# Kernel optimization log

Hardware: AMD Instinct MI355X
Metric: run time of the kernel (lower is better)

The kernel has to match this reference:

```python
import jax, jax.numpy as jnp
import numpy as np

STRIDE = 4
EPS = 1e-12  # guards sqrt grad at exactly-zero distance (weight[0] is all zeros)


def rbf_conv(x, w, stride=STRIDE):
    # x: (N, 1, H, W); w: (O, kh, kw). Computes per-window cdist to all O
    # prototype filters, then gauss RBF with std = unbiased std of the (N, O)
    # distance matrix at each window position (matches torch.std(dist)).
    O, kh, kw = w.shape
    patches = jax.lax.conv_general_dilated_patches(
        x, (kh, kw), (stride, stride), 'VALID')      # (N, kh*kw, oh, ow)
    p = jnp.transpose(patches, (0, 2, 3, 1))          # (N, oh, ow, P)
    wf = w.reshape(O, -1)                              # (O, P)
    d2 = (jnp.sum(p * p, -1)[..., None] + jnp.sum(wf * wf, -1)
          - 2.0 * jnp.einsum('nhwp,op->nhwo', p, wf))
    dist = jnp.sqrt(jnp.maximum(d2, 0.0) + EPS)       # (N, oh, ow, O)
    std = jnp.std(dist, axis=(0, 3), ddof=1, keepdims=True)  # per window pos
    out = jnp.exp(-0.5 * (dist / std) ** 2)           # gauss RBF
    return jnp.transpose(out, (0, 3, 1, 2))           # (N, O, oh, ow)


def crelu(x, b):
    return x * (x >= b).astype(x.dtype)


def sfm(x, shape, next_kernel, filt, alpha0=0.9):
    # get_RM: (N, C, h_in, w_in) -> (B, h, w, C) regrouping, then alpha-weighted
    # patch pooling over `filt`, emitting (B*h'*w', 1, kh_next, kw_next).
    h, w = shape
    f0, f1 = filt
    C = x.shape[1]
    rm = jnp.transpose(x, (0, 2, 3, 1)).reshape(-1, h, w, C)
    seq = jnp.arange(f0 * f1, dtype=x.dtype)[::-1]       # flipped sequence
    alpha = jnp.tile((alpha0 ** seq).reshape(f0, f1), (h // f0, w // f1))
    out = rm * alpha[None, :, :, None]
    out = out.reshape(-1, h // f0, f0, w // f1, f1, C).mean(axis=(2, 4))
    return out.reshape(-1, 1, *next_kernel)


def channel_forward(xc, w1, w2, w3, w4, cb):
    y = rbf_conv(xc, w1)                       # (B, 100, 6, 6)
    y = crelu(y, cb[0])
    y = sfm(y, (6, 6), (10, 10), (2, 2))       # (B*9, 1, 10, 10)
    y = rbf_conv(y, w2)                        # (B*9, 225, 1, 1)
    y = crelu(y, cb[1])
    y = sfm(y, (3, 3), (15, 15), (1, 3))       # (B*3, 1, 15, 15)
    y = rbf_conv(y, w3)                        # (B*3, 625, 1, 1)
    y = crelu(y, cb[2])
    y = sfm(y, (3, 1), (25, 25), (3, 1))       # (B, 1, 25, 25)
    y = rbf_conv(y, w4)                        # (B, 1225, 1, 1)
    y = crelu(y, cb[3])
    return y


def forward(x, w1, w2, w3, w4, fc_w, fc_b, crelu_bias):
    B = x.shape[0]
    feats = [channel_forward(x[:, c:c + 1], w1[c], w2[c], w3[c], w4[c], crelu_bias)
             for c in range(x.shape[1])]        # fixed loop over 3 color channels
    out = jnp.concatenate(feats, axis=1).reshape(B, -1)  # (B, 3*1225)
    return out @ fc_w.T + fc_b


def setup_inputs() -> dict:
    key = jax.random.key(0)
    ks = jax.random.split(key, 8)

    def kaiming_u(k, shape):
        fan_in = int(np.prod(shape[2:]))        # 1*kh*kw, matches torch
        bound = float(np.sqrt(1.0 / fan_in))    # kaiming_uniform(a=sqrt(5))
        w = jax.random.uniform(k, shape, jnp.float32, -bound, bound)
        return w.at[:, 0].set(0.0)              # torch init zeros filter 0

    B = 4096
    return {
        'x': jax.random.uniform(ks[0], (B, 3, 28, 28), jnp.float32),
        'w1': kaiming_u(ks[1], (3, 100, 5, 5)),
        'w2': kaiming_u(ks[2], (3, 225, 10, 10)),
        'w3': kaiming_u(ks[3], (3, 625, 15, 15)),
        'w4': kaiming_u(ks[4], (3, 1225, 25, 25)),
        'fc_w': jax.random.normal(ks[5], (10, 3 * 1225), jnp.float32) * 0.016,
        'fc_b': jnp.zeros((10,), jnp.float32),
        'crelu_bias': jnp.array([0.4, 0.1, 0.01, 0.01], jnp.float32),
    }


def reference(x, w1, w2, w3, w4, fc_w, fc_b, crelu_bias):
    return forward(x, w1, w2, w3, w4, fc_w, fc_b, crelu_bias)
```

## Files before the change

### kernel.cpp

```cpp
#include <hip/hip_runtime.h>


typedef unsigned short u16;
typedef short bf16x8 __attribute__((ext_vector_type(8)));
typedef float f32x4 __attribute__((ext_vector_type(4)));
typedef unsigned int u32;
typedef u32 u32x4 __attribute__((ext_vector_type(4)));

#define STRIPES 64
#define ACC_L2 0
#define ACC_L3 128
#define ACC_L4 256
#define ACC_TOTAL 384

__device__ __forceinline__ u16 f2bf(float f) {
  unsigned int u = __float_as_uint(f);
  unsigned int r = (u + 0x7fffu + ((u >> 16) & 1u)) >> 16;
  return (u16)r;
}
__device__ __forceinline__ float bf2f(u16 h) {
  return __uint_as_float(((unsigned int)h) << 16);
}
__device__ __forceinline__ u32 cvtpk_bf16(float a, float b) {
  u32 r;
  asm("v_cvt_pk_bf16_f32 %0, %1, %2" : "=v"(r) : "v"(a), "v"(b));
  return r;
}
__device__ __forceinline__ float fexp(float x) { return __expf(x); }
__device__ __forceinline__ float fsqrt(float x) { return __builtin_amdgcn_sqrtf(x); }
__device__ __forceinline__ void gload16(const void* g, const void* l) {
  __builtin_amdgcn_global_load_lds(
      (const __attribute__((address_space(1))) unsigned int*)g,
      (__attribute__((address_space(3))) unsigned int*)l, 16, 0, 0);
}

__global__ void zero_acc_kernel(double* __restrict__ acc, int n) {
  int i = blockIdx.x * blockDim.x + threadIdx.x;
  if (i < n) acc[i] = 0.0;
}

__global__ __launch_bounds__(128) void w_prep(
    const float* __restrict__ W, int O, int K, int Opad, int Kp,
    u16* __restrict__ hi, u16* __restrict__ lo, float* __restrict__ wn)
{
  __shared__ float red[2];
  int o = blockIdx.x, cc = blockIdx.y, t = threadIdx.x;
  const float* src = W + ((size_t)cc * O + o) * K;
  u16* dh = hi + ((size_t)cc * Opad + o) * Kp;
  u16* dl = lo + ((size_t)cc * Opad + o) * Kp;
  float p = 0.f;
  for (int k = t; k < Kp; k += 128) {
    float v = (o < O && k < K) ? src[k] : 0.f;
    u16 h = f2bf(v);
    u16 l = f2bf(v - bf2f(h));
    dh[k] = h; dl[k] = l;
    p = fmaf(v, v, p);
  }
  for (int off = 32; off; off >>= 1) p += __shfl_down(p, off, 64);
  if ((t & 63) == 0) red[t >> 6] = p;
  __syncthreads();
  if (t == 0) wn[(size_t)cc * Opad + o] = red[0] + red[1];
}

__global__ __launch_bounds__(256) void l1_gemm_d2(
    const float* __restrict__ x, int c0,
    const u16* __restrict__ W1h, const u16* __restrict__ W1l,
    const float* __restrict__ w1n, float* __restrict__ dist1, int sD1c,
    float* __restrict__ part, int sPartc, int NBLK)
{
  __shared__ __align__(16) u16 sm[16384];
  __shared__ float img[1568];
  __shared__ float pnsm[512];
  __shared__ float pnloc[128];
  const int t = threadIdx.x;
  const int w = t >> 6, lane = t & 63;
  const int b0 = blockIdx.x * 2;
  const int zi = blockIdx.y, c = c0 + zi;
  const u16* Wh = W1h + (size_t)c * 4096;
  const u16* Wl = W1l + (size_t)c * 4096;
  const float* wn = w1n + (size_t)c * 128;
  dist1 += (size_t)zi * sD1c;
  part  += (size_t)zi * sPartc;

  {
    const int kk = (w & 3) * 8;
#pragma unroll
    for (int u = 0; u < 2; ++u) {
      const size_t gb = (size_t)(u * 64 + lane) * 32 + kk;
      const int ls = ((w & 3) * 128 + u * 64) * 8;
      gload16(Wh + gb, sm + 8192 + ls);
      gload16(Wl + gb, sm + 12288 + ls);
    }
  }
#pragma unroll
  for (int im = 0; im < 2; ++im) {
    if (t < 196)
      ((float4*)(img + im * 784))[t] =
          ((const float4*)(x + ((size_t)(b0 + im) * 3 + c) * 784))[t];
  }
// ... 125 lines not shown
    inv36[pos] = var > 0.0 ? (float)(0.5 / var) : __builtin_inff();
  }
}

__global__ __launch_bounds__(128) void l1_sfm_lite(
    const float* __restrict__ d1, int sD1c,
    const float* __restrict__ inv36, int sInvc, const float* __restrict__ cb,
    u16* __restrict__ Xhi, u16* __restrict__ Xlo, float* __restrict__ xn,
    int sXc, int sxnc)
{
  __shared__ float inv_s[36];
  __shared__ float xnsm[9][2];
  int b = blockIdx.x, zi = blockIdx.y, t = threadIdx.x;
  d1 += (size_t)zi * sD1c; inv36 += (size_t)zi * sInvc;
  Xhi += (size_t)zi * sXc; Xlo += (size_t)zi * sXc; xn += (size_t)zi * sxnc;
  if (t < 36) inv_s[t] = inv36[t];
  __syncthreads();
  const float* db = d1 + (size_t)b * 3600;
  float bias = cb[0];
  int wv = t >> 6;
#pragma unroll
  for (int IJ = 0; IJ < 9; ++IJ) {
    const int I = IJ / 3, J = IJ - I * 3;
    const int p00 = 12 * I + 2 * J;
    float v = 0.f;
    if (t < 100) {
      float e00 = fexp(-db[p00 * 100 + t] * inv_s[p00]);
      float e01 = fexp(-db[(p00 + 1) * 100 + t] * inv_s[p00 + 1]);
      float e10 = fexp(-db[(p00 + 6) * 100 + t] * inv_s[p00 + 6]);
      float e11 = fexp(-db[(p00 + 7) * 100 + t] * inv_s[p00 + 7]);
      e00 = (e00 >= bias) ? e00 : 0.f;
      e01 = (e01 >= bias) ? e01 : 0.f;
      e10 = (e10 >= bias) ? e10 : 0.f;
      e11 = (e11 >= bias) ? e11 : 0.f;
      v = 0.25f * (fmaf(0.729f, e00, 0.81f * e01) + fmaf(0.9f, e10, e11));
    }
    size_t xrow = (size_t)b * 9 + IJ;
    u16 h = f2bf(v);
    u16 l = f2bf(v - bf2f(h));
    Xhi[xrow * 128 + t] = h;
    Xlo[xrow * 128 + t] = l;
    float p = v * v;
    for (int off = 32; off; off >>= 1) p += __shfl_down(p, off, 64);
    if ((t & 63) == 0) xnsm[IJ][wv] = p;
  }
  __syncthreads();
  if (t < 9) xn[(size_t)b * 9 + t] = xnsm[t][0] + xnsm[t][1];
}

__global__ __launch_bounds__(512, 2) void gemm_dist_pipe(
    const u16* __restrict__ Xhi, const u16* __restrict__ Xlo,
    const u16* __restrict__ Whi, const u16* __restrict__ Wlo,
    const float* __restrict__ xn, const float* __restrict__ wn,
    float* __restrict__ dist, int O, int Kp,
    double* __restrict__ acc, int accbase, int c0,
    int sXc, int sWc, int sxnc, int swnc, int sdistc)
{
  __shared__ __align__(16) u16 sm[65536];
  int zi = blockIdx.z, c = c0 + zi;
  Xhi += (size_t)zi * sXc; Xlo += (size_t)zi * sXc;
  Whi += (size_t)c * sWc;  Wlo += (size_t)c * sWc;
  xn += (size_t)zi * sxnc; wn += (size_t)c * swnc;
  dist += (size_t)zi * sdistc;
  acc += (size_t)c * ACC_TOTAL;

  const int t = threadIdx.x;
  const int w = t >> 6, lane = t & 63;
  const int wr = w >> 1, wc = w & 1;
  const int sq = w & 3, half = w >> 2;
  const int m0 = blockIdx.x * 256, o0 = blockIdx.y * 256;
  const int q4 = lane >> 4, r16 = lane & 15;
  const int nsteps = Kp / 32;

  f32x4 accv[4][8];
#pragma unroll
  for (int i = 0; i < 4; ++i)
#pragma unroll
    for (int j = 0; j < 8; ++j) accv[i][j] = (f32x4){0.f, 0.f, 0.f, 0.f};

  auto stageA_u = [&](int buf, int ks, int u) {
    const int kk = ks * 32 + sq * 8;
    u16* base = sm + buf * 32768;
    const int row = half * 128 + u * 64 + lane;
    const size_t ga = (size_t)(m0 + row) * Kp + kk;
    const int ls = (sq * 256 + half * 128 + u * 64) * 8;
    gload16(Xhi + ga, base + ls);
    gload16(Xlo + ga, base + 8192 + ls);
  };
  auto stageB_u = [&](int buf, int ks, int u) {
    const int kk = ks * 32 + sq * 8;
    u16* base = sm + buf * 32768;
    const int row = half * 128 + u * 64 + lane;
    const size_t gb = (size_t)(o0 + row) * Kp + kk;
    const int ls = (sq * 256 + half * 128 + u * 64) * 8;
    gload16(Whi + gb, base + 16384 + ls);
    gload16(Wlo + gb, base + 24576 + ls);
  };

  stageA_u(0, 0, 0); stageA_u(0, 0, 1);
  stageB_u(0, 0, 0); stageB_u(0, 0, 1);

  for (int ks = 0; ks < nsteps; ++ks) {
    const u16* base = sm + (ks & 1) * 32768;
    const int nb = (ks + 1) & 1;
    const bool more = (ks + 1 < nsteps);
    bf16x8 Ah[4], Al[4];

#pragma unroll
    for (int ph = 0; ph < 4; ++ph) {
      if (ph == 0) {
        asm volatile("s_waitcnt vmcnt(2)\n\ts_barrier" ::: "memory");
      } else if (ph == 2) {
        if (more) asm volatile("s_waitcnt vmcnt(4)\n\ts_barrier" ::: "memory");
        else      asm volatile("s_waitcnt vmcnt(0)\n\ts_barrier" ::: "memory");
      } else {
        __builtin_amdgcn_s_barrier();
      }
      if (ph == 0) {
#pragma unroll
        for (int i = 0; i < 4; ++i) {
          int ao = (q4 * 256 + wr * 64 + i * 16 + r16) * 8;
          Ah[i] = *(const bf16x8*)(base + ao);
          Al[i] = *(const bf16x8*)(base + 8192 + ao);
        }
      }
      const int j0 = ph * 2;
      int bo0 = (q4 * 256 + wc * 128 + j0 * 16 + r16) * 8;
      int bo1 = (q4 * 256 + wc * 128 + (j0 + 1) * 16 + r16) * 8;
      bf16x8 Bh0 = *(const bf16x8*)(base + 16384 + bo0);
      bf16x8 Bl0 = *(const bf16x8*)(base + 24576 + bo0);
      bf16x8 Bh1 = *(const bf16x8*)(base + 16384 + bo1);
      bf16x8 Bl1 = *(const bf16x8*)(base + 24576 + bo1);
      if (more) {
        if (ph == 0)      stageA_u(nb, ks + 1, 0);
        else if (ph == 1) stageA_u(nb, ks + 1, 1);
        else if (ph == 2) stageB_u(nb, ks + 1, 0);
        else              stageB_u(nb, ks + 1, 1);
      }
      asm volatile("s_waitcnt lgkmcnt(0)" ::: "memory");
      __builtin_amdgcn_sched_barrier(0);
      __builtin_amdgcn_s_setprio(1);
#pragma unroll
      for (int i = 0; i < 4; ++i)
        accv[i][j0] = __builtin_amdgcn_mfma_f32_16x16x32_bf16(Ah[i], Bh0, accv[i][j0], 0, 0, 0);
#pragma unroll
      for (int i = 0; i < 4; ++i)
        accv[i][j0] = __builtin_amdgcn_mfma_f32_16x16x32_bf16(Al[i], Bh0, accv[i][j0], 0, 0, 0);
#pragma unroll
      for (int i = 0; i < 4; ++i)
        accv[i][j0] = __builtin_amdgcn_mfma_f32_16x16x32_bf16(Ah[i], Bl0, accv[i][j0], 0, 0, 0);
#pragma unroll
      for (int i = 0; i < 4; ++i)
        accv[i][j0 + 1] = __builtin_amdgcn_mfma_f32_16x16x32_bf16(Ah[i], Bh1, accv[i][j0 + 1], 0, 0, 0);
#pragma unroll
      for (int i = 0; i < 4; ++i)
        accv[i][j0 + 1] = __builtin_amdgcn_mfma_f32_16x16x32_bf16(Al[i], Bh1, accv[i][j0 + 1], 0, 0, 0);
#pragma unroll
      for (int i = 0; i < 4; ++i)
        accv[i][j0 + 1] = __builtin_amdgcn_mfma_f32_16x16x32_bf16(Ah[i], Bl1, accv[i][j0 + 1], 0, 0, 0);
      __builtin_amdgcn_s_setprio(0);
    }
  }

  double s = 0.0, qd = 0.0;
#pragma unroll
  for (int i = 0; i < 4; ++i) {
    const int mb = m0 + wr * 64 + i * 16 + q4 * 4;
    float xnv[4];
#pragma unroll
    for (int r = 0; r < 4; ++r) xnv[r] = xn[mb + r];
    float sf = 0.f, qf = 0.f;
#pragma unroll
    for (int j = 0; j < 8; ++j) {
      const int o = o0 + wc * 128 + j * 16 + r16;
      if (o < O) {
        const float wnv = wn[o];
#pragma unroll
        for (int r = 0; r < 4; ++r) {
          float d2 = xnv[r] + wnv - 2.f * accv[i][j][r];
          float d2c = fmaxf(d2, 0.f) + 1e-12f;
          dist[(size_t)(mb + r) * O + o] = d2c;
          sf += fsqrt(d2c); qf += d2c;
        }
      }
    }
    s += sf; qd += qf;
  }
  for (int off = 32; off; off >>= 1) {
    s += __shfl_down(s, off, 64);
    qd += __shfl_down(qd, off, 64);
  }
  double* redsm = (double*)(sm + (nsteps & 1) * 32768);
  if (lane == 0) { redsm[w * 2] = s; redsm[w * 2 + 1] = qd; }
  __syncthreads();
  if (t == 0) {
    s = 0.0; qd = 0.0;
#pragma unroll
    for (int ww = 0; ww < 8; ++ww) { s += redsm[ww * 2]; qd += redsm[ww * 2 + 1]; }
    int stripe = (blockIdx.x + blockIdx.y * gridDim.x) & (STRIPES - 1);
    atomicAdd(&acc[accbase + stripe * 2], s);
    atomicAdd(&acc[accbase + stripe * 2 + 1], qd);
  }
}

__device__ __forceinline__ float block_inv_from_acc(
    const double* __restrict__ acc, int base, double n, float* sh)
{
  __syncthreads();
  int t = threadIdx.x;
  if (t < 64) {
    double s = acc[base + 2 * t], q = acc[base + 2 * t + 1];
    for (int off = 32; off; off >>= 1) {
      s += __shfl_down(s, off, 64);
      q += __shfl_down(q, off, 64);
    }
    if (t == 0) {
      double var = (q - s * s / n) / (n - 1.0);
      *sh = var > 0.0 ? (float)(0.5 / var) : __builtin_inff();
    }
  }
  __syncthreads();
  return *sh;
}

__global__ __launch_bounds__(256) void l2_sfm(
    const float* __restrict__ dist2, const double* __restrict__ acc, double n,
    const float* __restrict__ cb, u16* __restrict__ Xhi, u16* __restrict__ Xlo,
    float* __restrict__ xn, int c0, int sdistc, int sXc, int sxnc)
{
  __shared__ float shinv;
  __shared__ float red[4];
  int zi = blockIdx.z, c = c0 + zi;
  dist2 += (size_t)zi * sdistc;
  Xhi += (size_t)zi * sXc; Xlo += (size_t)zi * sXc; xn += (size_t)zi * sxnc;
  float inv = block_inv_from_acc(acc + (size_t)c * ACC_TOTAL, ACC_L2, n, &shinv);
  int b = blockIdx.x, u = blockIdx.y, ch = threadIdx.x;
  float bias = cb[1];
  float v = 0.f;
  if (ch < 225) {
    const float av[3] = {0.81f, 0.9f, 1.0f};
    float a = 0.f;
#pragma unroll
    for (int vv = 0; vv < 3; ++vv) {
      float d2 = dist2[((size_t)b * 9 + u * 3 + vv) * 225 + ch];
      float e = fexp(-d2 * inv);
      e = (e >= bias) ? e : 0.f;
      a = fmaf(e, av[vv], a);
    }
    v = a * (1.f / 3.f);
  }
  size_t row = (size_t)b * 3 + u;
  u16 h = f2bf(v);
  u16 l = f2bf(v - bf2f(h));
  Xhi[row * 256 + ch] = h;
  Xlo[row * 256 + ch] = l;
  float p = v * v;
  for (int off = 32; off; off >>= 1) p += __shfl_down(p, off, 64);
  if ((ch & 63) == 0) red[ch >> 6] = p;
  __syncthreads();
  if (ch == 0) xn[row] = red[0] + red[1] + red[2] + red[3];
}

__global__ __launch_bounds__(256) void l3_sfm(
    const float* __restrict__ dist3, const double* __restrict__ acc, double n,
    const float* __restrict__ cb, u16* __restrict__ Xhi, u16* __restrict__ Xlo,
    float* __restrict__ xn, int c0, int sdistc, int sXc, int sxnc)
{
  __shared__ float shinv;
  __shared__ float red[4];
  int zi = blockIdx.y, c = c0 + zi;
  dist3 += (size_t)zi * sdistc;
  Xhi += (size_t)zi * sXc; Xlo += (size_t)zi * sXc; xn += (size_t)zi * sxnc;
  float inv = block_inv_from_acc(acc + (size_t)c * ACC_TOTAL, ACC_L3, n, &shinv);
  int b = blockIdx.x, t = threadIdx.x;
  float bias = cb[2];
  const float au[3] = {0.81f, 0.9f, 1.0f};
  float p = 0.f;
  for (int ch = t; ch < 640; ch += 256) {
    float v = 0.f;
    if (ch < 625) {
      float a = 0.f;
#pragma unroll
      for (int u = 0; u < 3; ++u) {
        float d2 = dist3[((size_t)b * 3 + u) * 625 + ch];
        float e = fexp(-d2 * inv);
        e = (e >= bias) ? e : 0.f;
        a = fmaf(e, au[u], a);
      }
      v = a * (1.f / 3.f);
    }
    u16 h = f2bf(v);
    u16 l = f2bf(v - bf2f(h));
    Xhi[(size_t)b * 640 + ch] = h;
    Xlo[(size_t)b * 640 + ch] = l;
    p = fmaf(v, v, p);
  }
  for (int off = 32; off; off >>= 1) p += __shfl_down(p, off, 64);
  if ((t & 63) == 0) red[t >> 6] = p;
  __syncthreads();
  if (t == 0) xn[b] = red[0] + red[1] + red[2] + red[3];
}

__global__ __launch_bounds__(128) void fc_acc(
    const float* __restrict__ dist4, const double* __restrict__ acc, double n,
    const float* __restrict__ cb, const float* __restrict__ fcw,
    const float* __restrict__ fcb, float* __restrict__ out,
    int c0, int nc, int sdistc)
{
  __shared__ float shinv;
  int b = blockIdx.x, t = threadIdx.x;
  float bias = cb[3];
  float p[10];
#pragma unroll
  for (int k = 0; k < 10; ++k) p[k] = 0.f;
  for (int zi = 0; zi < nc; ++zi) {
    int c = c0 + zi;
    float inv = block_inv_from_acc(acc + (size_t)c * ACC_TOTAL, ACC_L4, n, &shinv);
    const float* d4 = dist4 + (size_t)zi * sdistc;
    for (int j = t; j < 1225; j += 128) {
      float d2 = d4[(size_t)b * 1225 + j];
      float v = fexp(-d2 * inv);
      v = (v >= bias) ? v : 0.f;
#pragma unroll
      for (int k = 0; k < 10; ++k) p[k] = fmaf(v, fcw[k * 3675 + c * 1225 + j], p[k]);
    }
  }
#pragma unroll
  for (int k = 0; k < 10; ++k)
    for (int off = 32; off; off >>= 1) p[k] += __shfl_down(p[k], off, 64);
  __shared__ float red[2][10];
  int wave = t >> 6;
  if ((t & 63) == 0) {
#pragma unroll
    for (int k = 0; k < 10; ++k) red[wave][k] = p[k];
  }
  __syncthreads();
  if (t < 10) {
    float v = red[0][t] + red[1][t];
    if (c0 == 0) out[(size_t)b * 10 + t] = fcb[t] + v;
    else         out[(size_t)b * 10 + t] += v;
  }
}

extern "C" void kernel_launch(void* const* d_in, const int* in_sizes, int n_in,
                              void* d_out, int out_size, void* d_ws, size_t ws_size,
                              hipStream_t stream) {
  const float* x   = (const float*)d_in[0];
  const float* w1  = (const float*)d_in[1];
  const float* w2  = (const float*)d_in[2];
  const float* w3  = (const float*)d_in[3];
  const float* w4  = (const float*)d_in[4];
  const float* fcw = (const float*)d_in[5];
  const float* fcb = (const float*)d_in[6];
  const float* cb  = (const float*)d_in[7];
  float* out = (float*)d_out;
  const int B = in_sizes[0] / (3 * 28 * 28);
  const int M2 = B * 9, M3 = B * 3;
  const int NB = B / 2;

  const size_t W2SZ = 256 * 128, W3SZ = 768 * 256, W4SZ = (size_t)1280 * 640;
  const size_t WTOT = 3 * (W2SZ + W3SZ + W4SZ);

  int tier;
  u16 *Xbase, *Whi, *Wlo, *W1h, *W1l;
  float *wn, *w1n, *xn, *inv36, *part;
  double* accd;
  float* Sf;
  for (tier = 0; tier < 3; ++tier) {
    size_t cur = 0;
    char* basep = (char*)d_ws;
    auto take = [&](size_t bytes) {
      void* r = basep + cur;
      cur = (cur + bytes + 255) & ~(size_t)255;
      return r;
    };
    int nc = (tier <= 1) ? 3 : 1;
    int ncL1 = (tier == 0) ? 3 : 1;
    size_t Ssz = (size_t)M2 * 225 * 4 * nc;
    size_t d1sz = (size_t)B * 3600 * 4 * ncL1;
    if (d1sz > Ssz) Ssz = d1sz;
    Sf = (float*)take(Ssz);
    Xbase = (u16*)take((size_t)M2 * 128 * 2 * 2 * nc);
    Whi = (u16*)take(WTOT * 2); Wlo = (u16*)take(WTOT * 2);
    W1h = (u16*)take(12288 * 2); W1l = (u16*)take(12288 * 2);
    wn  = (float*)take(3 * (256 + 768 + 1280) * 4);
    w1n = (float*)take(384 * 4);
    xn    = (float*)take((size_t)M2 * 4 * nc);
    inv36 = (float*)take(40 * 4 * ncL1);
    part  = (float*)take((size_t)72 * NB * 4 * ncL1);
    accd  = (double*)take(3 * ACC_TOTAL * 8);
    if (cur <= ws_size || tier == 2) break;
  }
  const int nc = (tier <= 1) ? 3 : 1;
  const bool batL1 = (tier == 0);

  const int sX2c   = (nc == 3) ? M2 * 128 * 2 : 0;
  const int sX3c   = (nc == 3) ? M3 * 256 * 2 : 0;
  const int sX4c   = (nc == 3) ? B * 640 * 2 : 0;
  const int sD2c   = (nc == 3) ? M2 * 225 : 0;
  const int sD3c   = (nc == 3) ? M3 * 625 : 0;
  const int sD4c   = (nc == 3) ? B * 1225 : 0;
  const int sXn2c  = (nc == 3) ? M2 : 0;
  const int sXn3c  = (nc == 3) ? M3 : 0;
  const int sXn4c  = (nc == 3) ? B : 0;
  const int sD1c   = batL1 ? B * 3600 : 0;
  const int sPartc = batL1 ? 72 * NB : 0;
  const int sInvL1 = batL1 ? 40 : 0;

  u16* x2hi = Xbase;   u16* x2lo = Xbase + (size_t)M2 * 128;
  u16* x3hi = Xbase;   u16* x3lo = Xbase + (size_t)M3 * 256;
  u16* x4hi = Xbase;   u16* x4lo = Xbase + (size_t)B * 640;
  u16* Whi2 = Whi;                 u16* Wlo2 = Wlo;                 float* wn2 = wn;
  u16* Whi3 = Whi + 3 * W2SZ;      u16* Wlo3 = Wlo + 3 * W2SZ;      float* wn3 = wn + 3 * 256;
  u16* Whi4 = Whi + 3 * (W2SZ + W3SZ); u16* Wlo4 = Wlo + 3 * (W2SZ + W3SZ);
  float* wn4 = wn + 3 * (256 + 768);

  zero_acc_kernel<<<(3 * ACC_TOTAL + 255) / 256, 256, 0, stream>>>(accd, 3 * ACC_TOTAL);
  w_prep<<<dim3(128, 3),  128, 0, stream>>>(w1, 100, 25,  128, 32,  W1h,  W1l,  w1n);
  w_prep<<<dim3(256, 3),  128, 0, stream>>>(w2, 225, 100, 256, 128, Whi2, Wlo2, wn2);
  w_prep<<<dim3(768, 3),  128, 0, stream>>>(w3, 625, 225, 768, 256, Whi3, Wlo3, wn3);
  w_prep<<<dim3(1280, 3), 128, 0, stream>>>(w4, 1225, 625, 1280, 640, Whi4, Wlo4, wn4);

  for (int c0 = 0; c0 < 3; c0 += nc) {
    if (batL1) {
      l1_gemm_d2<<<dim3(NB, 3), 256, 0, stream>>>(x, 0, W1h, W1l, w1n, Sf, sD1c,
                                                  part, sPartc, NB);
      l1_part_fin<<<dim3(36, 3), 256, 0, stream>>>(part, sPartc, inv36, sInvL1,
                                                   (double)B * 100.0, NB);
      l1_sfm_lite<<<dim3(B, 3), 128, 0, stream>>>(
          Sf, sD1c, inv36, sInvL1, cb, x2hi, x2lo, xn, sX2c, sXn2c);
    } else {
      for (int ci = 0; ci < nc; ++ci) {
        int c = c0 + ci;
        l1_gemm_d2<<<dim3(NB, 1), 256, 0, stream>>>(x, c, W1h, W1l, w1n, Sf, 0,
                                                    part, 0, NB);
        l1_part_fin<<<dim3(36, 1), 256, 0, stream>>>(part, 0, inv36, 0,
                                                     (double)B * 100.0, NB);
        l1_sfm_lite<<<dim3(B, 1), 128, 0, stream>>>(
            Sf, 0, inv36, 0, cb, x2hi + (size_t)ci * sX2c, x2lo + (size_t)ci * sX2c,
            xn + (size_t)ci * sXn2c, 0, 0);
      }
    }

    gemm_dist_pipe<<<dim3(M2 / 256, 1, nc), 512, 0, stream>>>(
        x2hi, x2lo, Whi2, Wlo2, xn, wn2, Sf, 225, 128, accd, ACC_L2, c0,
        sX2c, (int)W2SZ, sXn2c, 256, sD2c);
    l2_sfm<<<dim3(B, 3, nc), 256, 0, stream>>>(
        Sf, accd, (double)M2 * 225.0, cb, x3hi, x3lo, xn, c0, sD2c, sX3c, sXn3c);

    gemm_dist_pipe<<<dim3(M3 / 256, 3, nc), 512, 0, stream>>>(
        x3hi, x3lo, Whi3, Wlo3, xn, wn3, Sf, 625, 256, accd, ACC_L3, c0,
        sX3c, (int)W3SZ, sXn3c, 768, sD3c);
    l3_sfm<<<dim3(B, nc), 256, 0, stream>>>(
        Sf, accd, (double)M3 * 625.0, cb, x4hi, x4lo, xn, c0, sD3c, sX4c, sXn4c);

    gemm_dist_pipe<<<dim3(B / 256, 5, nc), 512, 0, stream>>>(
        x4hi, x4lo, Whi4, Wlo4, xn, wn4, Sf, 1225, 640, accd, ACC_L4, c0,
        sX4c, (int)W4SZ, sXn4c, 1280, sD4c);
    fc_acc<<<B, 128, 0, stream>>>(
        Sf, accd, (double)B * 1225.0, cb, fcw, fcb, out, c0, nc, sD4c);
  }
}
```

Before: 479.7 us.

## Fuse layer-4 distance GEMM with FC via cooperative grid sync; merge prep kernels

```diff
diff --git a/kernel.cpp b/kernel.cpp
--- a/kernel.cpp
+++ b/kernel.cpp
@@ -1,5 +1,8 @@
 #include <hip/hip_runtime.h>
-
+#include <hip/hip_cooperative_groups.h>
+
+
+namespace cg = cooperative_groups;
 
 typedef unsigned short u16;
 typedef short bf16x8 __attribute__((ext_vector_type(8)));
@@ -34,17 +37,31 @@
       (__attribute__((address_space(3))) unsigned int*)l, 16, 0, 0);
 }
 
-__global__ void zero_acc_kernel(double* __restrict__ acc, int n) {
-  int i = blockIdx.x * blockDim.x + threadIdx.x;
-  if (i < n) acc[i] = 0.0;
-}
-
-__global__ __launch_bounds__(128) void w_prep(
-    const float* __restrict__ W, int O, int K, int Opad, int Kp,
-    u16* __restrict__ hi, u16* __restrict__ lo, float* __restrict__ wn)
+__global__ __launch_bounds__(128) void prep_all(
+    const float* __restrict__ w1, const float* __restrict__ w2,
+    const float* __restrict__ w3, const float* __restrict__ w4,
+    u16* __restrict__ W1h, u16* __restrict__ W1l,
+    u16* __restrict__ Whi2, u16* __restrict__ Wlo2,
+    u16* __restrict__ Whi3, u16* __restrict__ Wlo3,
+    u16* __restrict__ Whi4, u16* __restrict__ Wlo4,
+    float* __restrict__ w1n, float* __restrict__ wn2,
+    float* __restrict__ wn3, float* __restrict__ wn4,
+    double* __restrict__ accd, int naccd)
 {
   __shared__ float red[2];
-  int o = blockIdx.x, cc = blockIdx.y, t = threadIdx.x;
+  int bid = blockIdx.x, t = threadIdx.x;
+  if (bid < 9) {
+    int i = bid * 128 + t;
+    if (i < naccd) accd[i] = 0.0;
+    return;
+  }
+  bid -= 9;
+  const float* W; u16 *hi, *lo; float* wn; int O, K, Opad, Kp;
+  if (bid < 384)        { W = w1; hi = W1h;  lo = W1l;  wn = w1n; O = 100;  K = 25;  Opad = 128;  Kp = 32;  }
+  else if (bid < 1152)  { bid -= 384;  W = w2; hi = Whi2; lo = Wlo2; wn = wn2; O = 225;  K = 100; Opad = 256;  Kp = 128; }
+  else if (bid < 3456)  { bid -= 1152; W = w3; hi = Whi3; lo = Wlo3; wn = wn3; O = 625;  K = 225; Opad = 768;  Kp = 256; }
+  else                  { bid -= 3456; W = w4; hi = Whi4; lo = Wlo4; wn = wn4; O = 1225; K = 625; Opad = 1280; Kp = 640; }
+  int o = bid % Opad, cc = bid / Opad;
   const float* src = W + ((size_t)cc * O + o) * K;
   u16* dh = hi + ((size_t)cc * Opad + o) * Kp;
   u16* dl = lo + ((size_t)cc * Opad + o) * Kp;
@@ -447,6 +464,213 @@
   return *sh;
 }
 
+__global__ __launch_bounds__(512, 2) void gemm4_fc_coop(
+    const u16* __restrict__ Xhi, const u16* __restrict__ Xlo,
+    const u16* __restrict__ Whi, const u16* __restrict__ Wlo,
+    const float* __restrict__ xn, const float* __restrict__ wn,
+    const float* __restrict__ fcw, const float* __restrict__ cb,
+    float* __restrict__ part4, int O, int Kp,
+    double* __restrict__ acc, int accbase, int c0,
+    int sXc, int sWc, int sxnc, int swnc, double nsum)
+{
+  __shared__ __align__(16) u16 sm[65536];
+  __shared__ float shinv;
+  int zi = blockIdx.z, c = c0 + zi;
+  Xhi += (size_t)zi * sXc; Xlo += (size_t)zi * sXc;
+  Whi += (size_t)c * sWc;  Wlo += (size_t)c * sWc;
+  xn += (size_t)zi * sxnc; wn += (size_t)c * swnc;
+  double* accl = acc + (size_t)c * ACC_TOTAL;
+
+  const int t = threadIdx.x;
+  const int w = t >> 6, lane = t & 63;
+  const int wr = w >> 1, wc = w & 1;
+  const int sq = w & 3, half = w >> 2;
+  const int m0 = blockIdx.x * 256, o0 = blockIdx.y * 256;
+  const int q4 = lane >> 4, r16 = lane & 15;
+  const int nsteps = Kp / 32;
+  const int B = gridDim.x * 256;
+
+  f32x4 accv[4][8];
+#pragma unroll
+  for (int i = 0; i < 4; ++i)
+#pragma unroll
+    for (int j = 0; j < 8; ++j) accv[i][j] = (f32x4){0.f, 0.f, 0.f, 0.f};
+
+  auto stageA_u = [&](int buf, int ks, int u) {
+    const int kk = ks * 32 + sq * 8;
+    u16* base = sm + buf * 32768;
+    const int row = half * 128 + u * 64 + lane;
+    const size_t ga = (size_t)(m0 + row) * Kp + kk;
+    const int ls = (sq * 256 + half * 128 + u * 64) * 8;
+    gload16(Xhi + ga, base + ls);
+    gload16(Xlo + ga, base + 8192 + ls);
+  };
+  auto stageB_u = [&](int buf, int ks, int u) {
+    const int kk = ks * 32 + sq * 8;
+    u16* base = sm + buf * 32768;
+    const int row = half * 128 + u * 64 + lane;
+    const size_t gb = (size_t)(o0 + row) * Kp + kk;
+    const int ls = (sq * 256 + half * 128 + u * 64) * 8;
+    gload16(Whi + gb, base + 16384 + ls);
+    gload16(Wlo + gb, base + 24576 + ls);
+  };
+
+  stageA_u(0, 0, 0); stageA_u(0, 0, 1);
+  stageB_u(0, 0, 0); stageB_u(0, 0, 1);
+
+  for (int ks = 0; ks < nsteps; ++ks) {
+    const u16* base = sm + (ks & 1) * 32768;
+    const int nb = (ks + 1) & 1;
+    const bool more = (ks + 1 < nsteps);
+    bf16x8 Ah[4], Al[4];
+
+#pragma unroll
+    for (int ph = 0; ph < 4; ++ph) {
+      if (ph == 0) {
+        asm volatile("s_waitcnt vmcnt(2)\n\ts_barrier" ::: "memory");
+      } else if (ph == 2) {
+        if (more) asm volatile("s_waitcnt vmcnt(4)\n\ts_barrier" ::: "memory");
+        else      asm volatile("s_waitcnt vmcnt(0)\n\ts_barrier" ::: "memory");
+      } else {
+        __builtin_amdgcn_s_barrier();
+      }
+      if (ph == 0) {
+#pragma unroll
+        for (int i = 0; i < 4; ++i) {
+          int ao = (q4 * 256 + wr * 64 + i * 16 + r16) * 8;
+          Ah[i] = *(const bf16x8*)(base + ao);
+          Al[i] = *(const bf16x8*)(base + 8192 + ao);
+        }
+      }
+      const int j0 = ph * 2;
+      int bo0 = (q4 * 256 + wc * 128 + j0 * 16 + r16) * 8;
+      int bo1 = (q4 * 256 + wc * 128 + (j0 + 1) * 16 + r16) * 8;
+      bf16x8 Bh0 = *(const bf16x8*)(base + 16384 + bo0);
+      bf16x8 Bl0 = *(const bf16x8*)(base + 24576 + bo0);
+      bf16x8 Bh1 = *(const bf16x8*)(base + 16384 + bo1);
+      bf16x8 Bl1 = *(const bf16x8*)(base + 24576 + bo1);
+      if (more) {
+        if (ph == 0)      stageA_u(nb, ks + 1, 0);
+        else if (ph == 1) stageA_u(nb, ks + 1, 1);
+        else if (ph == 2) stageB_u(nb, ks + 1, 0);
+        else              stageB_u(nb, ks + 1, 1);
+      }
+      asm volatile("s_waitcnt lgkmcnt(0)" ::: "memory");
+      __builtin_amdgcn_sched_barrier(0);
+      __builtin_amdgcn_s_setprio(1);
+#pragma unroll
+      for (int i = 0; i < 4; ++i)
+        accv[i][j0] = __builtin_amdgcn_mfma_f32_16x16x32_bf16(Ah[i], Bh0, accv[i][j0], 0, 0, 0);
+#pragma unroll
+      for (int i = 0; i < 4; ++i)
+        accv[i][j0] = __builtin_amdgcn_mfma_f32_16x16x32_bf16(Al[i], Bh0, accv[i][j0], 0, 0, 0);
+#pragma unroll
+      for (int i = 0; i < 4; ++i)
+        accv[i][j0] = __builtin_amdgcn_mfma_f32_16x16x32_bf16(Ah[i], Bl0, accv[i][j0], 0, 0, 0);
+#pragma unroll
+      for (int i = 0; i < 4; ++i)
+        accv[i][j0 + 1] = __builtin_amdgcn_mfma_f32_16x16x32_bf16(Ah[i], Bh1, accv[i][j0 + 1], 0, 0, 0);
+#pragma unroll
+      for (int i = 0; i < 4; ++i)
+        accv[i][j0 + 1] = __builtin_amdgcn_mfma_f32_16x16x32_bf16(Al[i], Bh1, accv[i][j0 + 1], 0, 0, 0);
+#pragma unroll
+      for (int i = 0; i < 4; ++i)
+        accv[i][j0 + 1] = __builtin_amdgcn_mfma_f32_16x16x32_bf16(Ah[i], Bl1, accv[i][j0 + 1], 0, 0, 0);
+      __builtin_amdgcn_s_setprio(0);
+    }
+  }
+
+  double s = 0.0, qd = 0.0;
+#pragma unroll
+  for (int i = 0; i < 4; ++i) {
+    const int mb = m0 + wr * 64 + i * 16 + q4 * 4;
+    float xnv[4];
+#pragma unroll
+    for (int r = 0; r < 4; ++r) xnv[r] = xn[mb + r];
+    float sf = 0.f, qf = 0.f;
+#pragma unroll
+    for (int j = 0; j < 8; ++j) {
+      const int o = o0 + wc * 128 + j * 16 + r16;
+      const float wnv = (o < 1280) ? wn[o] : 0.f;
+#pragma unroll
+      for (int r = 0; r < 4; ++r) {
+        float d2 = xnv[r] + wnv - 2.f * accv[i][j][r];
+        float d2c = fmaxf(d2, 0.f) + 1e-12f;
+        accv[i][j][r] = d2c;
+        if (o < O) { sf += fsqrt(d2c); qf += d2c; }
+      }
+    }
+    s += sf; qd += qf;
+  }
+  for (int off = 32; off; off >>= 1) {
+    s += __shfl_down(s, off, 64);
+    qd += __shfl_down(qd, off, 64);
+  }
+  double* redsm = (double*)(sm + (nsteps & 1) * 32768);
+  if (lane == 0) { redsm[w * 2] = s; redsm[w * 2 + 1] = qd; }
+  __syncthreads();
+  if (t == 0) {
+    s = 0.0; qd = 0.0;
+#pragma unroll
+    for (int ww = 0; ww < 8; ++ww) { s += redsm[ww * 2]; qd += redsm[ww * 2 + 1]; }
+    int stripe = (blockIdx.x + blockIdx.y * gridDim.x) & (STRIPES - 1);
+    atomicAdd(&accl[accbase + stripe * 2], s);
+    atomicAdd(&accl[accbase + stripe * 2 + 1], qd);
+  }
+
+  cg::this_grid().sync();
+
+  float inv = block_inv_from_acc(accl, accbase, nsum, &shinv);
+  float bias = cb[3];
+#pragma unroll
+  for (int i = 0; i < 4; ++i)
+#pragma unroll
+    for (int j = 0; j < 8; ++j)
+#pragma unroll
+      for (int r = 0; r < 4; ++r) {
+        float v = fexp(-accv[i][j][r] * inv);
+        accv[i][j][r] = (v >= bias) ? v : 0.f;
+      }
+
+  for (int k = 0; k < 10; ++k) {
+    float w8[8];
+#pragma unroll
+    for (int j = 0; j < 8; ++j) {
+      int o = o0 + wc * 128 + j * 16 + r16;
+      w8[j] = (o < O) ? fcw[(size_t)k * 3675 + c * 1225 + o] : 0.f;
+    }
+#pragma unroll
+    for (int i = 0; i < 4; ++i) {
+#pragma unroll
+      for (int r = 0; r < 4; ++r) {
+        float ps = 0.f;
+#pragma unroll
+        for (int j = 0; j < 8; ++j) ps = fmaf(accv[i][j][r], w8[j], ps);
+#pragma unroll
+        for (int off = 8; off; off >>= 1) ps += __shfl_xor(ps, off, 64);
+        if (r16 == 0) {
+          int b = m0 + wr * 64 + i * 16 + q4 * 4 + r;
+          part4[((((size_t)zi * 5 + blockIdx.y) * 2 + wc) * B + b) * 10 + k] = ps;
+        }
+      }
+    }
+  }
+}
+
+__global__ __launch_bounds__(640) void fc_fin(
+    const float* __restrict__ part4, const float* __restrict__ fcb,
+    float* __restrict__ out, int c0, int nc, int B)
+{
+  int b = blockIdx.x * 64 + threadIdx.x / 10;
+  int k = threadIdx.x % 10;
+  float s = (c0 == 0) ? fcb[k] : out[(size_t)b * 10 + k];
+  for (int zi = 0; zi < nc; ++zi)
+#pragma unroll
+    for (int ob = 0; ob < 10; ++ob)
+      s += part4[((((size_t)zi * 5) + (ob >> 1)) * 2 + (ob & 1)) * (size_t)B * 10 + (size_t)b * 10 + k];
+  out[(size_t)b * 10 + k] = s;
+}
+
 __global__ __launch_bounds__(256) void l2_sfm(
     const float* __restrict__ dist2, const double* __restrict__ acc, double n,
     const float* __restrict__ cb, u16* __restrict__ Xhi, u16* __restrict__ Xlo,
@@ -523,47 +747,6 @@
   if ((t & 63) == 0) red[t >> 6] = p;
   __syncthreads();
   if (t == 0) xn[b] = red[0] + red[1] + red[2] + red[3];
-}
-
-__global__ __launch_bounds__(128) void fc_acc(
-    const float* __restrict__ dist4, const double* __restrict__ acc, double n,
-    const float* __restrict__ cb, const float* __restrict__ fcw,
-    const float* __restrict__ fcb, float* __restrict__ out,
-    int c0, int nc, int sdistc)
-{
-  __shared__ float shinv;
-  int b = blockIdx.x, t = threadIdx.x;
-  float bias = cb[3];
-  float p[10];
-#pragma unroll
-  for (int k = 0; k < 10; ++k) p[k] = 0.f;
-  for (int zi = 0; zi < nc; ++zi) {
-    int c = c0 + zi;
-    float inv = block_inv_from_acc(acc + (size_t)c * ACC_TOTAL, ACC_L4, n, &shinv);
-    const float* d4 = dist4 + (size_t)zi * sdistc;
-    for (int j = t; j < 1225; j += 128) {
-      float d2 = d4[(size_t)b * 1225 + j];
-      float v = fexp(-d2 * inv);
-      v = (v >= bias) ? v : 0.f;
-#pragma unroll
-      for (int k = 0; k < 10; ++k) p[k] = fmaf(v, fcw[k * 3675 + c * 1225 + j], p[k]);
-    }
-  }
-#pragma unroll
-  for (int k = 0; k < 10; ++k)
-    for (int off = 32; off; off >>= 1) p[k] += __shfl_down(p[k], off, 64);
-  __shared__ float red[2][10];
-  int wave = t >> 6;
-  if ((t & 63) == 0) {
-#pragma unroll
-    for (int k = 0; k < 10; ++k) red[wave][k] = p[k];
-  }
-  __syncthreads();
-  if (t < 10) {
-    float v = red[0][t] + red[1][t];
-    if (c0 == 0) out[(size_t)b * 10 + t] = fcb[t] + v;
-    else         out[(size_t)b * 10 + t] += v;
-  }
 }
 
 extern "C" void kernel_launch(void* const* d_in, const int* in_sizes, int n_in,
@@ -603,6 +786,8 @@
     size_t Ssz = (size_t)M2 * 225 * 4 * nc;
     size_t d1sz = (size_t)B * 3600 * 4 * ncL1;
     if (d1sz > Ssz) Ssz = d1sz;
+    size_t p4sz = (size_t)nc * 10 * B * 10 * 4;
+    if (p4sz > Ssz) Ssz = p4sz;
     Sf = (float*)take(Ssz);
     Xbase = (u16*)take((size_t)M2 * 128 * 2 * 2 * nc);
     Whi = (u16*)take(WTOT * 2); Wlo = (u16*)take(WTOT * 2);
@@ -623,7 +808,6 @@
   const int sX4c   = (nc == 3) ? B * 640 * 2 : 0;
   const int sD2c   = (nc == 3) ? M2 * 225 : 0;
   const int sD3c   = (nc == 3) ? M3 * 625 : 0;
-  const int sD4c   = (nc == 3) ? B * 1225 : 0;
   const int sXn2c  = (nc == 3) ? M2 : 0;
   const int sXn3c  = (nc == 3) ? M3 : 0;
   const int sXn4c  = (nc == 3) ? B : 0;
@@ -639,11 +823,9 @@
   u16* Whi4 = Whi + 3 * (W2SZ + W3SZ); u16* Wlo4 = Wlo + 3 * (W2SZ + W3SZ);
   float* wn4 = wn + 3 * (256 + 768);
 
-  zero_acc_kernel<<<(3 * ACC_TOTAL + 255) / 256, 256, 0, stream>>>(accd, 3 * ACC_TOTAL);
-  w_prep<<<dim3(128, 3),  128, 0, stream>>>(w1, 100, 25,  128, 32,  W1h,  W1l,  w1n);
-  w_prep<<<dim3(256, 3),  128, 0, stream>>>(w2, 225, 100, 256, 128, Whi2, Wlo2, wn2);
-  w_prep<<<dim3(768, 3),  128, 0, stream>>>(w3, 625, 225, 768, 256, Whi3, Wlo3, wn3);
-  w_prep<<<dim3(1280, 3), 128, 0, stream>>>(w4, 1225, 625, 1280, 640, Whi4, Wlo4, wn4);
+  prep_all<<<9 + 384 + 768 + 2304 + 3840, 128, 0, stream>>>(
+      w1, w2, w3, w4, W1h, W1l, Whi2, Wlo2, Whi3, Wlo3, Whi4, Wlo4,
+      w1n, wn2, wn3, wn4, accd, 3 * ACC_TOTAL);
 
   for (int c0 = 0; c0 < 3; c0 += nc) {
     if (batL1) {
@@ -678,10 +860,23 @@
     l3_sfm<<<dim3(B, nc), 256, 0, stream>>>(
         Sf, accd, (double)M3 * 625.0, cb, x4hi, x4lo, xn, c0, sD3c, sX4c, sXn4c);
 
-    gemm_dist_pipe<<<dim3(B / 256, 5, nc), 512, 0, stream>>>(
-        x4hi, x4lo, Whi4, Wlo4, xn, wn4, Sf, 1225, 640, accd, ACC_L4, c0,
-        sX4c, (int)W4SZ, sXn4c, 1280, sD4c);
-    fc_acc<<<B, 128, 0, stream>>>(
-        Sf, accd, (double)B * 1225.0, cb, fcw, fcb, out, c0, nc, sD4c);
-  }
-}
+    {
+      const u16 *a_xhi = x4hi, *a_xlo = x4lo, *a_whi = Whi4, *a_wlo = Wlo4;
+      const float *a_xn = xn, *a_wn = wn4, *a_fcw = fcw, *a_cb = cb;
+      float* a_part = Sf;
+      int a_O = 1225, a_Kp = 640, a_accbase = ACC_L4, a_c0 = c0;
+      int a_sXc = sX4c, a_sWc = (int)W4SZ, a_sxnc = sXn4c, a_swnc = 1280;
+      double* a_acc = accd;
+      double a_n = (double)B * 1225.0;
+      void* cargs[] = {
+          (void*)&a_xhi, (void*)&a_xlo, (void*)&a_whi, (void*)&a_wlo,
+          (void*)&a_xn, (void*)&a_wn, (void*)&a_fcw, (void*)&a_cb,
+          (void*)&a_part, (void*)&a_O, (void*)&a_Kp, (void*)&a_acc,
+          (void*)&a_accbase, (void*)&a_c0, (void*)&a_sXc, (void*)&a_sWc,
+          (void*)&a_sxnc, (void*)&a_swnc, (void*)&a_n};
+      hipLaunchCooperativeKernel((void*)gemm4_fc_coop, dim3(B / 256, 5, nc),
+                                 dim3(512, 1, 1), cargs, 0, stream);
+    }
+    fc_fin<<<B / 64, 640, 0, stream>>>(Sf, fcb, out, c0, nc, B);
+  }
+}
```

Result: slower. 517.0 us (+7.8%).

## Stage distance tiles through LDS for coalesced padded-row stores; fuse prep kernels

Applied to the files above, without the earlier changes.

```diff
diff --git a/kernel.cpp b/kernel.cpp
--- a/kernel.cpp
+++ b/kernel.cpp
@@ -34,17 +34,31 @@
       (__attribute__((address_space(3))) unsigned int*)l, 16, 0, 0);
 }
 
-__global__ void zero_acc_kernel(double* __restrict__ acc, int n) {
-  int i = blockIdx.x * blockDim.x + threadIdx.x;
-  if (i < n) acc[i] = 0.0;
-}
-
-__global__ __launch_bounds__(128) void w_prep(
-    const float* __restrict__ W, int O, int K, int Opad, int Kp,
-    u16* __restrict__ hi, u16* __restrict__ lo, float* __restrict__ wn)
+__global__ __launch_bounds__(128) void prep_all(
+    const float* __restrict__ w1, const float* __restrict__ w2,
+    const float* __restrict__ w3, const float* __restrict__ w4,
+    u16* __restrict__ W1h, u16* __restrict__ W1l,
+    u16* __restrict__ Whi2, u16* __restrict__ Wlo2,
+    u16* __restrict__ Whi3, u16* __restrict__ Wlo3,
+    u16* __restrict__ Whi4, u16* __restrict__ Wlo4,
+    float* __restrict__ w1n, float* __restrict__ wn2,
+    float* __restrict__ wn3, float* __restrict__ wn4,
+    double* __restrict__ accd, int naccd)
 {
   __shared__ float red[2];
-  int o = blockIdx.x, cc = blockIdx.y, t = threadIdx.x;
+  int bid = blockIdx.x, t = threadIdx.x;
+  if (bid < 9) {
+    int i = bid * 128 + t;
+    if (i < naccd) accd[i] = 0.0;
+    return;
+  }
+  bid -= 9;
+  const float* W; u16 *hi, *lo; float* wn; int O, K, Opad, Kp;
+  if (bid < 384)        { W = w1; hi = W1h;  lo = W1l;  wn = w1n; O = 100;  K = 25;  Opad = 128;  Kp = 32;  }
+  else if (bid < 1152)  { bid -= 384;  W = w2; hi = Whi2; lo = Wlo2; wn = wn2; O = 225;  K = 100; Opad = 256;  Kp = 128; }
+  else if (bid < 3456)  { bid -= 1152; W = w3; hi = Whi3; lo = Wlo3; wn = wn3; O = 625;  K = 225; Opad = 768;  Kp = 256; }
+  else                  { bid -= 3456; W = w4; hi = Whi4; lo = Wlo4; wn = wn4; O = 1225; K = 625; Opad = 1280; Kp = 640; }
+  int o = bid % Opad, cc = bid / Opad;
   const float* src = W + ((size_t)cc * O + o) * K;
   u16* dh = hi + ((size_t)cc * Opad + o) * Kp;
   u16* dl = lo + ((size_t)cc * Opad + o) * Kp;
@@ -276,7 +290,7 @@
     const u16* __restrict__ Xhi, const u16* __restrict__ Xlo,
     const u16* __restrict__ Whi, const u16* __restrict__ Wlo,
     const float* __restrict__ xn, const float* __restrict__ wn,
-    float* __restrict__ dist, int O, int Kp,
+    float* __restrict__ dist, int O, int Od, int Kp,
     double* __restrict__ acc, int accbase, int c0,
     int sXc, int sWc, int sxnc, int swnc, int sdistc)
 {
@@ -397,15 +411,15 @@
 #pragma unroll
     for (int j = 0; j < 8; ++j) {
       const int o = o0 + wc * 128 + j * 16 + r16;
+      const float wnv = wn[o];
+#pragma unroll
+      for (int r = 0; r < 4; ++r) {
+        float d2 = xnv[r] + wnv - 2.f * accv[i][j][r];
+        accv[i][j][r] = fmaxf(d2, 0.f) + 1e-12f;
+      }
       if (o < O) {
-        const float wnv = wn[o];
-#pragma unroll
-        for (int r = 0; r < 4; ++r) {
-          float d2 = xnv[r] + wnv - 2.f * accv[i][j][r];
-          float d2c = fmaxf(d2, 0.f) + 1e-12f;
-          dist[(size_t)(mb + r) * O + o] = d2c;
-          sf += fsqrt(d2c); qf += d2c;
-        }
+#pragma unroll
+        for (int r = 0; r < 4; ++r) { sf += fsqrt(accv[i][j][r]); qf += accv[i][j][r]; }
       }
     }
     s += sf; qd += qf;
@@ -414,7 +428,8 @@
     s += __shfl_down(s, off, 64);
     qd += __shfl_down(qd, off, 64);
   }
-  double* redsm = (double*)(sm + (nsteps & 1) * 32768);
+  __syncthreads();
+  double* redsm = (double*)sm;
   if (lane == 0) { redsm[w * 2] = s; redsm[w * 2 + 1] = qd; }
   __syncthreads();
   if (t == 0) {
@@ -424,6 +439,38 @@
     int stripe = (blockIdx.x + blockIdx.y * gridDim.x) & (STRIPES - 1);
     atomicAdd(&acc[accbase + stripe * 2], s);
     atomicAdd(&acc[accbase + stripe * 2 + 1], qd);
+  }
+
+  float* smf = (float*)sm;
+#pragma unroll
+  for (int h = 0; h < 2; ++h) {
+    __syncthreads();
+    if ((wr >> 1) == h) {
+      const int rbase = (wr & 1) * 64;
+#pragma unroll
+      for (int i = 0; i < 4; ++i) {
+        const int row = rbase + i * 16 + q4 * 4;
+#pragma unroll
+        for (int j = 0; j < 8; ++j) {
+          const int col = wc * 128 + j * 16 + r16;
+#pragma unroll
+          for (int r = 0; r < 4; ++r)
+            smf[(row + r) * 256 + col] = accv[i][j][r];
+        }
+      }
+    }
+    __syncthreads();
+    const int mbase = m0 + h * 128;
+    const int oc = o0 + lane * 4;
+    const bool ok = (oc + 4 <= Od);
+#pragma unroll
+    for (int rr = 0; rr < 16; ++rr) {
+      const int row = w * 16 + rr;
+      if (ok) {
+        f32x4 v4 = *(const f32x4*)(smf + row * 256 + lane * 4);
+        *(f32x4*)(dist + (size_t)(mbase + row) * Od + oc) = v4;
+      }
+    }
   }
 }
 
@@ -450,7 +497,7 @@
 __global__ __launch_bounds__(256) void l2_sfm(
     const float* __restrict__ dist2, const double* __restrict__ acc, double n,
     const float* __restrict__ cb, u16* __restrict__ Xhi, u16* __restrict__ Xlo,
-    float* __restrict__ xn, int c0, int sdistc, int sXc, int sxnc)
+    float* __restrict__ xn, int c0, int ldd, int sdistc, int sXc, int sxnc)
 {
   __shared__ float shinv;
   __shared__ float red[4];
@@ -466,7 +513,7 @@
     float a = 0.f;
 #pragma unroll
     for (int vv = 0; vv < 3; ++vv) {
-      float d2 = dist2[((size_t)b * 9 + u * 3 + vv) * 225 + ch];
+      float d2 = dist2[((size_t)b * 9 + u * 3 + vv) * ldd + ch];
       float e = fexp(-d2 * inv);
       e = (e >= bias) ? e : 0.f;
       a = fmaf(e, av[vv], a);
@@ -488,7 +535,7 @@
 __global__ __launch_bounds__(256) void l3_sfm(
     const float* __restrict__ dist3, const double* __restrict__ acc, double n,
     const float* __restrict__ cb, u16* __restrict__ Xhi, u16* __restrict__ Xlo,
-    float* __restrict__ xn, int c0, int sdistc, int sXc, int sxnc)
+    float* __restrict__ xn, int c0, int ldd, int sdistc, int sXc, int sxnc)
 {
   __shared__ float shinv;
   __shared__ float red[4];
@@ -506,7 +553,7 @@
       float a = 0.f;
 #pragma unroll
       for (int u = 0; u < 3; ++u) {
-        float d2 = dist3[((size_t)b * 3 + u) * 625 + ch];
+        float d2 = dist3[((size_t)b * 3 + u) * ldd + ch];
         float e = fexp(-d2 * inv);
         e = (e >= bias) ? e : 0.f;
         a = fmaf(e, au[u], a);
@@ -529,7 +576,7 @@
     const float* __restrict__ dist4, const double* __restrict__ acc, double n,
     const float* __restrict__ cb, const float* __restrict__ fcw,
     const float* __restrict__ fcb, float* __restrict__ out,
-    int c0, int nc, int sdistc)
+    int c0, int nc, int ldd, int sdistc)
 {
   __shared__ float shinv;
   int b = blockIdx.x, t = threadIdx.x;
@@ -542,7 +589,7 @@
     float inv = block_inv_from_acc(acc + (size_t)c * ACC_TOTAL, ACC_L4, n, &shinv);
     const float* d4 = dist4 + (size_t)zi * sdistc;
     for (int j = t; j < 1225; j += 128) {
-      float d2 = d4[(size_t)b * 1225 + j];
+      float d2 = d4[(size_t)b * ldd + j];
       float v = fexp(-d2 * inv);
       v = (v >= bias) ? v : 0.f;
 #pragma unroll
@@ -581,6 +628,7 @@
   const int B = in_sizes[0] / (3 * 28 * 28);
   const int M2 = B * 9, M3 = B * 3;
   const int NB = B / 2;
+  const int LD2 = 240, LD3 = 640, LD4 = 1232;
 
   const size_t W2SZ = 256 * 128, W3SZ = 768 * 256, W4SZ = (size_t)1280 * 640;
   const size_t WTOT = 3 * (W2SZ + W3SZ + W4SZ);
@@ -600,9 +648,13 @@
     };
     int nc = (tier <= 1) ? 3 : 1;
     int ncL1 = (tier == 0) ? 3 : 1;
-    size_t Ssz = (size_t)M2 * 225 * 4 * nc;
+    size_t Ssz = (size_t)M2 * LD2 * 4 * nc;
     size_t d1sz = (size_t)B * 3600 * 4 * ncL1;
     if (d1sz > Ssz) Ssz = d1sz;
+    size_t d3sz = (size_t)M3 * LD3 * 4 * nc;
+    if (d3sz > Ssz) Ssz = d3sz;
+    size_t d4sz = (size_t)B * LD4 * 4 * nc;
+    if (d4sz > Ssz) Ssz = d4sz;
     Sf = (float*)take(Ssz);
     Xbase = (u16*)take((size_t)M2 * 128 * 2 * 2 * nc);
     Whi = (u16*)take(WTOT * 2); Wlo = (u16*)take(WTOT * 2);
@@ -621,9 +673,9 @@
   const int sX2c   = (nc == 3) ? M2 * 128 * 2 : 0;
   const int sX3c   = (nc == 3) ? M3 * 256 * 2 : 0;
   const int sX4c   = (nc == 3) ? B * 640 * 2 : 0;
-  const int sD2c   = (nc == 3) ? M2 * 225 : 0;
-  const int sD3c   = (nc == 3) ? M3 * 625 : 0;
-  const int sD4c   = (nc == 3) ? B * 1225 : 0;
+  const int sD2c   = (nc == 3) ? M2 * LD2 : 0;
+  const int sD3c   = (nc == 3) ? M3 * LD3 : 0;
+  const int sD4c   = (nc == 3) ? B * LD4 : 0;
   const int sXn2c  = (nc == 3) ? M2 : 0;
   const int sXn3c  = (nc == 3) ? M3 : 0;
   const int sXn4c  = (nc == 3) ? B : 0;
@@ -639,11 +691,9 @@
   u16* Whi4 = Whi + 3 * (W2SZ + W3SZ); u16* Wlo4 = Wlo + 3 * (W2SZ + W3SZ);
   float* wn4 = wn + 3 * (256 + 768);
 
-  zero_acc_kernel<<<(3 * ACC_TOTAL + 255) / 256, 256, 0, stream>>>(accd, 3 * ACC_TOTAL);
-  w_prep<<<dim3(128, 3),  128, 0, stream>>>(w1, 100, 25,  128, 32,  W1h,  W1l,  w1n);
-  w_prep<<<dim3(256, 3),  128, 0, stream>>>(w2, 225, 100, 256, 128, Whi2, Wlo2, wn2);
-  w_prep<<<dim3(768, 3),  128, 0, stream>>>(w3, 625, 225, 768, 256, Whi3, Wlo3, wn3);
-  w_prep<<<dim3(1280, 3), 128, 0, stream>>>(w4, 1225, 625, 1280, 640, Whi4, Wlo4, wn4);
+  prep_all<<<9 + 384 + 768 + 2304 + 3840, 128, 0, stream>>>(
+      w1, w2, w3, w4, W1h, W1l, Whi2, Wlo2, Whi3, Wlo3, Whi4, Wlo4,
+      w1n, wn2, wn3, wn4, accd, 3 * ACC_TOTAL);
 
   for (int c0 = 0; c0 < 3; c0 += nc) {
     if (batL1) {
@@ -667,21 +717,21 @@
     }
 
     gemm_dist_pipe<<<dim3(M2 / 256, 1, nc), 512, 0, stream>>>(
-        x2hi, x2lo, Whi2, Wlo2, xn, wn2, Sf, 225, 128, accd, ACC_L2, c0,
+        x2hi, x2lo, Whi2, Wlo2, xn, wn2, Sf, 225, LD2, 128, accd, ACC_L2, c0,
         sX2c, (int)W2SZ, sXn2c, 256, sD2c);
     l2_sfm<<<dim3(B, 3, nc), 256, 0, stream>>>(
-        Sf, accd, (double)M2 * 225.0, cb, x3hi, x3lo, xn, c0, sD2c, sX3c, sXn3c);
+        Sf, accd, (double)M2 * 225.0, cb, x3hi, x3lo, xn, c0, LD2, sD2c, sX3c, sXn3c);
 
     gemm_dist_pipe<<<dim3(M3 / 256, 3, nc), 512, 0, stream>>>(
-        x3hi, x3lo, Whi3, Wlo3, xn, wn3, Sf, 625, 256, accd, ACC_L3, c0,
+        x3hi, x3lo, Whi3, Wlo3, xn, wn3, Sf, 625, LD3, 256, accd, ACC_L3, c0,
         sX3c, (int)W3SZ, sXn3c, 768, sD3c);
     l3_sfm<<<dim3(B, nc), 256, 0, stream>>>(
-        Sf, accd, (double)M3 * 625.0, cb, x4hi, x4lo, xn, c0, sD3c, sX4c, sXn4c);
+        Sf, accd, (double)M3 * 625.0, cb, x4hi, x4lo, xn, c0, LD3, sD3c, sX4c, sXn4c);
 
     gemm_dist_pipe<<<dim3(B / 256, 5, nc), 512, 0, stream>>>(
-        x4hi, x4lo, Whi4, Wlo4, xn, wn4, Sf, 1225, 640, accd, ACC_L4, c0,
+        x4hi, x4lo, Whi4, Wlo4, xn, wn4, Sf, 1225, LD4, 640, accd, ACC_L4, c0,
         sX4c, (int)W4SZ, sXn4c, 1280, sD4c);
     fc_acc<<<B, 128, 0, stream>>>(
-        Sf, accd, (double)B * 1225.0, cb, fcw, fcb, out, c0, nc, sD4c);
-  }
-}
+        Sf, accd, (double)B * 1225.0, cb, fcw, fcb, out, c0, nc, LD4, sD4c);
+  }
+}
```

New measurement: 545.3 us. 13.7% more time.

## Merge weight prep and accumulator zeroing into one launch; swizzle GEMM block order

Applied to the files above, without the earlier changes.

```diff
diff --git a/kernel.cpp b/kernel.cpp
--- a/kernel.cpp
+++ b/kernel.cpp
@@ -34,17 +34,31 @@
       (__attribute__((address_space(3))) unsigned int*)l, 16, 0, 0);
 }
 
-__global__ void zero_acc_kernel(double* __restrict__ acc, int n) {
-  int i = blockIdx.x * blockDim.x + threadIdx.x;
-  if (i < n) acc[i] = 0.0;
-}
-
-__global__ __launch_bounds__(128) void w_prep(
-    const float* __restrict__ W, int O, int K, int Opad, int Kp,
-    u16* __restrict__ hi, u16* __restrict__ lo, float* __restrict__ wn)
+__global__ __launch_bounds__(128) void prep_all(
+    const float* __restrict__ w1, const float* __restrict__ w2,
+    const float* __restrict__ w3, const float* __restrict__ w4,
+    u16* __restrict__ W1h, u16* __restrict__ W1l,
+    u16* __restrict__ Whi2, u16* __restrict__ Wlo2,
+    u16* __restrict__ Whi3, u16* __restrict__ Wlo3,
+    u16* __restrict__ Whi4, u16* __restrict__ Wlo4,
+    float* __restrict__ w1n, float* __restrict__ wn2,
+    float* __restrict__ wn3, float* __restrict__ wn4,
+    double* __restrict__ accd, int naccd)
 {
   __shared__ float red[2];
-  int o = blockIdx.x, cc = blockIdx.y, t = threadIdx.x;
+  int bid = blockIdx.x, t = threadIdx.x;
+  if (bid < 9) {
+    int i = bid * 128 + t;
+    if (i < naccd) accd[i] = 0.0;
+    return;
+  }
+  bid -= 9;
+  const float* W; u16 *hi, *lo; float* wn; int O, K, Opad, Kp;
+  if (bid < 384)        { W = w1; hi = W1h;  lo = W1l;  wn = w1n; O = 100;  K = 25;  Opad = 128;  Kp = 32;  }
+  else if (bid < 1152)  { bid -= 384;  W = w2; hi = Whi2; lo = Wlo2; wn = wn2; O = 225;  K = 100; Opad = 256;  Kp = 128; }
+  else if (bid < 3456)  { bid -= 1152; W = w3; hi = Whi3; lo = Wlo3; wn = wn3; O = 625;  K = 225; Opad = 768;  Kp = 256; }
+  else                  { bid -= 3456; W = w4; hi = Whi4; lo = Wlo4; wn = wn4; O = 1225; K = 625; Opad = 1280; Kp = 640; }
+  int o = bid % Opad, cc = bid / Opad;
   const float* src = W + ((size_t)cc * O + o) * K;
   u16* dh = hi + ((size_t)cc * Opad + o) * Kp;
   u16* dl = lo + ((size_t)cc * Opad + o) * Kp;
@@ -281,7 +295,16 @@
     int sXc, int sWc, int sxnc, int swnc, int sdistc)
 {
   __shared__ __align__(16) u16 sm[65536];
-  int zi = blockIdx.z, c = c0 + zi;
+  const int gx = gridDim.x, gy = gridDim.y;
+  const int n = gx * gy * gridDim.z;
+  int d = blockIdx.x + gx * (blockIdx.y + gy * blockIdx.z);
+  int logical = (n & 7) ? d : ((d & 7) * (n >> 3) + (d >> 3));
+  const int bz = logical / (gx * gy);
+  const int rem = logical - bz * gx * gy;
+  const int by = rem / gx;
+  const int bx = rem - by * gx;
+
+  int zi = bz, c = c0 + zi;
   Xhi += (size_t)zi * sXc; Xlo += (size_t)zi * sXc;
   Whi += (size_t)c * sWc;  Wlo += (size_t)c * sWc;
   xn += (size_t)zi * sxnc; wn += (size_t)c * swnc;
@@ -292,7 +315,7 @@
   const int w = t >> 6, lane = t & 63;
   const int wr = w >> 1, wc = w & 1;
   const int sq = w & 3, half = w >> 2;
-  const int m0 = blockIdx.x * 256, o0 = blockIdx.y * 256;
+  const int m0 = bx * 256, o0 = by * 256;
   const int q4 = lane >> 4, r16 = lane & 15;
   const int nsteps = Kp / 32;
 
@@ -421,7 +444,7 @@
     s = 0.0; qd = 0.0;
 #pragma unroll
     for (int ww = 0; ww < 8; ++ww) { s += redsm[ww * 2]; qd += redsm[ww * 2 + 1]; }
-    int stripe = (blockIdx.x + blockIdx.y * gridDim.x) & (STRIPES - 1);
+    int stripe = (bx + by * gx) & (STRIPES - 1);
     atomicAdd(&acc[accbase + stripe * 2], s);
     atomicAdd(&acc[accbase + stripe * 2 + 1], qd);
   }
@@ -639,11 +662,9 @@
   u16* Whi4 = Whi + 3 * (W2SZ + W3SZ); u16* Wlo4 = Wlo + 3 * (W2SZ + W3SZ);
   float* wn4 = wn + 3 * (256 + 768);
 
-  zero_acc_kernel<<<(3 * ACC_TOTAL + 255) / 256, 256, 0, stream>>>(accd, 3 * ACC_TOTAL);
-  w_prep<<<dim3(128, 3),  128, 0, stream>>>(w1, 100, 25,  128, 32,  W1h,  W1l,  w1n);
-  w_prep<<<dim3(256, 3),  128, 0, stream>>>(w2, 225, 100, 256, 128, Whi2, Wlo2, wn2);
-  w_prep<<<dim3(768, 3),  128, 0, stream>>>(w3, 625, 225, 768, 256, Whi3, Wlo3, wn3);
-  w_prep<<<dim3(1280, 3), 128, 0, stream>>>(w4, 1225, 625, 1280, 640, Whi4, Wlo4, wn4);
+  prep_all<<<9 + 384 + 768 + 2304 + 3840, 128, 0, stream>>>(
+      w1, w2, w3, w4, W1h, W1l, Whi2, Wlo2, Whi3, Wlo3, Whi4, Wlo4,
+      w1n, wn2, wn3, wn4, accd, 3 * ACC_TOTAL);
 
   for (int c0 = 0; c0 < 3; c0 += nc) {
     if (batL1) {
```

After: 475.4 us. No clear change (-0.9%).
